# Optimization experiments

Measured on AMD Instinct MI355X. Metric: run time of the kernel, lower is better.

The kernel has to match this reference:

```python
import jax, jax.numpy as jnp
import numpy as np

D = 64
H = 4
HD = D // H
N_MOL, E_MOL = 2048, 32768
N_PROT, E_PROT = 8192, 262144
LN_EPS = 1e-5


def _lin_params(key, d_in, d_out):
    k1, k2 = jax.random.split(key)
    lim = 1.0 / np.sqrt(d_in)
    w = jax.random.uniform(k1, (d_in, d_out), minval=-lim, maxval=lim, dtype=jnp.float32)
    b = jax.random.uniform(k2, (d_out,), minval=-lim, maxval=lim, dtype=jnp.float32)
    return w, b


def setup_inputs() -> dict:
    key = jax.random.key(0)
    ks = jax.random.split(key, 20)
    inp = {
        'x_mol': jax.random.normal(ks[0], (N_MOL, D), dtype=jnp.float32),
        'edge_index_mol': jax.random.randint(ks[1], (2, E_MOL), 0, N_MOL),
        'edge_attr_mol': jax.random.normal(ks[2], (E_MOL, D), dtype=jnp.float32),
        'x_prot': jax.random.normal(ks[3], (N_PROT, D), dtype=jnp.float32),
        'edge_index_prot': jax.random.randint(ks[4], (2, E_PROT), 0, N_PROT),
        'edge_attr_prot': jax.random.normal(ks[5], (E_PROT, D), dtype=jnp.float32),
    }
    # GINE MLPs: Linear -> ReLU -> Linear
    inp['mol_w1'], inp['mol_b1'] = _lin_params(ks[6], D, D)
    inp['mol_w2'], inp['mol_b2'] = _lin_params(ks[7], D, D)
    inp['prot_w1'], inp['prot_b1'] = _lin_params(ks[8], D, D)
    inp['prot_w2'], inp['prot_b2'] = _lin_params(ks[9], D, D)
    # cross-attn mol->prot (query=mol, key/value=prot)
    inp['mp_wq'], inp['mp_bq'] = _lin_params(ks[10], D, D)
    inp['mp_wk'], inp['mp_bk'] = _lin_params(ks[11], D, D)
    inp['mp_wv'], inp['mp_bv'] = _lin_params(ks[12], D, D)
    # cross-attn prot->mol (query=prot, key/value=mol)
    inp['pm_wq'], inp['pm_bq'] = _lin_params(ks[13], D, D)
    inp['pm_wk'], inp['pm_bk'] = _lin_params(ks[14], D, D)
    inp['pm_wv'], inp['pm_bv'] = _lin_params(ks[15], D, D)
    # layer norms
    inp['ln_mol_g'] = jnp.ones((D,), jnp.float32)
    inp['ln_mol_b'] = jnp.zeros((D,), jnp.float32)
    inp['ln_prot_g'] = jnp.ones((D,), jnp.float32)
    inp['ln_prot_b'] = jnp.zeros((D,), jnp.float32)
    return inp


def _gine_conv(x, edge_index, edge_attr, w1, b1, w2, b2, n_nodes):
    # message: relu(x_j + edge_attr); aggregate: mean at target; update: MLP((1+eps)*x + aggr), eps=0
    src, dst = edge_index[0], edge_index[1]
    msg = jax.nn.relu(x[src] + edge_attr)                       # [E, D]
    ssum = jax.ops.segment_sum(msg, dst, num_segments=n_nodes)  # [N, D]
    cnt = jax.ops.segment_sum(jnp.ones((msg.shape[0],), msg.dtype), dst, num_segments=n_nodes)
    aggr = ssum / jnp.maximum(cnt, 1.0)[:, None]
    h = x + aggr
    h = jax.nn.relu(h @ w1 + b1) @ w2 + b2
    return h


def _cross_attn(q_nodes, k_nodes, wq, bq, wk, bk, wv, bv):
    Nq, Nk = q_nodes.shape[0], k_nodes.shape[0]
    Q = (q_nodes @ wq + bq).reshape(Nq, H, HD)
    K = (k_nodes @ wk + bk).reshape(Nk, H, HD)
    V = (k_nodes @ wv + bv).reshape(Nk, H, HD)
    scores = jnp.einsum('qhd,khd->hqk', Q, K) / np.sqrt(HD).astype(np.float32)
    attn = jax.nn.softmax(scores, axis=-1)                      # [H, Nq, Nk]
    out = jnp.einsum('hqk,khd->qhd', attn, V).reshape(Nq, D)
    return out


def _layer_norm(x, g, b):
    mu = jnp.mean(x, axis=-1, keepdims=True)
    var = jnp.mean(jnp.square(x - mu), axis=-1, keepdims=True)
    return (x - mu) * jax.lax.rsqrt(var + LN_EPS) * g + b


def reference(x_mol, edge_index_mol, edge_attr_mol, x_prot, edge_index_prot, edge_attr_prot,
              mol_w1, mol_b1, mol_w2, mol_b2, prot_w1, prot_b1, prot_w2, prot_b2,
              mp_wq, mp_bq, mp_wk, mp_bk, mp_wv, mp_bv,
              pm_wq, pm_bq, pm_wk, pm_bk, pm_wv, pm_bv,
              ln_mol_g, ln_mol_b, ln_prot_g, ln_prot_b):
    h_mol = jax.nn.relu(_gine_conv(x_mol, edge_index_mol, edge_attr_mol,
                                   mol_w1, mol_b1, mol_w2, mol_b2, x_mol.shape[0]))
    h_prot = jax.nn.relu(_gine_conv(x_prot, edge_index_prot, edge_attr_prot,
                                    prot_w1, prot_b1, prot_w2, prot_b2, x_prot.shape[0]))
    h_mol_attn = _cross_attn(h_mol, h_prot, mp_wq, mp_bq, mp_wk, mp_bk, mp_wv, mp_bv)
    h_prot_attn = _cross_attn(h_prot, h_mol, pm_wq, pm_bq, pm_wk, pm_bk, pm_wv, pm_bv)
    out_mol = _layer_norm(h_mol + h_mol_attn, ln_mol_g, ln_mol_b)
    out_prot = _layer_norm(h_prot + h_prot_attn, ln_prot_g, ln_prot_b)
    return out_mol, out_prot
```

## Files before the change

### kernel.cpp

```cpp
#include <hip/hip_runtime.h>

#define NM 2048
#define EM 32768
#define NP 8192
#define EP 262144

typedef __attribute__((ext_vector_type(8))) short short8;
typedef __attribute__((ext_vector_type(4))) float f32x4;

#define LOG2E 1.44269504088896340736f

__device__ __forceinline__ float e2(float x) { return __builtin_amdgcn_exp2f(x); }
__device__ __forceinline__ unsigned int pk_bf16_tr(float a, float b) {
    return __builtin_amdgcn_perm(__float_as_uint(a), __float_as_uint(b), 0x03020706u);
}
__device__ __forceinline__ unsigned short cvt_bf16(float f) {
    unsigned int u = __float_as_uint(f);
    u = (u + 0x7fff + ((u >> 16) & 1)) >> 16;
    return (unsigned short)u;
}

__global__ __launch_bounds__(256) void hist_kernel(
    const int* __restrict__ ei_m, const int* __restrict__ ei_p,
    int* __restrict__ cnt_m, int* __restrict__ cnt_p)
{
    int idx = blockIdx.x * 256 + threadIdx.x;
    if (idx < EM) atomicAdd(&cnt_m[ei_m[EM + idx]], 1);
    int j = idx - EM;
    if (j >= 0 && j < EP) atomicAdd(&cnt_p[ei_p[EP + j]], 1);
}

__global__ __launch_bounds__(256) void scan_kernel(
    const int* __restrict__ cnt_m, const int* __restrict__ cnt_p,
    int* __restrict__ start_m, int* __restrict__ start_p,
    int* __restrict__ cur_m, int* __restrict__ cur_p)
{
    const int* cnt; int* start; int* cur; int n;
    if (blockIdx.x == 0) { cnt = cnt_m; start = start_m; cur = cur_m; n = NM; }
    else                 { cnt = cnt_p; start = start_p; cur = cur_p; n = NP; }
    int per = n >> 8;
    int tid = threadIdx.x;
    int base = tid * per;
    int s = 0;
    for (int i = 0; i < per; i++) s += cnt[base + i];
    __shared__ int wsum[4];
    int lane = tid & 63, w = tid >> 6;
    int v = s;
    #pragma unroll
    for (int off = 1; off < 64; off <<= 1) {
        int u = __shfl_up(v, off, 64);
        if (lane >= off) v += u;
    }
    if (lane == 63) wsum[w] = v;
    __syncthreads();
    int wo = 0;
    for (int i = 0; i < w; i++) wo += wsum[i];
    int run = wo + v - s;
    for (int i = 0; i < per; i++) {
        start[base + i] = run; cur[base + i] = run;
        run += cnt[base + i];
    }
    if (tid == 255) start[n] = run;
}

__global__ __launch_bounds__(256) void scatter_kernel(
    const int* __restrict__ ei_m, const int* __restrict__ ei_p,
    int* __restrict__ cur_m, int* __restrict__ cur_p,
    int* __restrict__ pidx_m, int* __restrict__ pidx_p)
{
    int idx = blockIdx.x * 256 + threadIdx.x;
    if (idx < EM) {
        int d = ei_m[EM + idx];
        int pos = atomicAdd(&cur_m[d], 1);
        pidx_m[pos] = (idx << 11) | ei_m[idx];
    }
    int j = idx - EM;
    if (j >= 0 && j < EP) {
        int d = ei_p[EP + j];
        int pos = atomicAdd(&cur_p[d], 1);
        pidx_p[pos] = (j << 13) | ei_p[j];
    }
}

__global__ __launch_bounds__(256) void node_aggr_kernel(
    const float* __restrict__ x_m, const float* __restrict__ ea_m,
    const int* __restrict__ start_m, const int* __restrict__ pidx_m,
    const float* __restrict__ x_p, const float* __restrict__ ea_p,
    const int* __restrict__ start_p, const int* __restrict__ pidx_p,
    float* __restrict__ h0_m, float* __restrict__ h0_p)
{
    int wave = threadIdx.x >> 6, lane = threadIdx.x & 63;
    int nid = blockIdx.x * 4 + wave;
    const float *x, *ea; const int *start, *pidx; float* h0; int n, sh, msk;
    if (nid < NM) { x = x_m; ea = ea_m; start = start_m; pidx = pidx_m; h0 = h0_m; n = nid; sh = 11; msk = 2047; }
    else          { x = x_p; ea = ea_p; start = start_p; pidx = pidx_p; h0 = h0_p; n = nid - NM; sh = 13; msk = 8191; }
    int b  = __builtin_amdgcn_readfirstlane(start[n]);
    int e  = __builtin_amdgcn_readfirstlane(start[n + 1]);
    int deg = e - b;
    const int* pp = pidx + b;
    float acc = 0.f;
    int j = 0;
    for (; j + 8 <= deg; j += 8) {
        int v0 = __builtin_amdgcn_readfirstlane(pp[j]);
        int v1 = __builtin_amdgcn_readfirstlane(pp[j + 1]);
        int v2 = __builtin_amdgcn_readfirstlane(pp[j + 2]);
        int v3 = __builtin_amdgcn_readfirstlane(pp[j + 3]);
        int v4 = __builtin_amdgcn_readfirstlane(pp[j + 4]);
        int v5 = __builtin_amdgcn_readfirstlane(pp[j + 5]);
        int v6 = __builtin_amdgcn_readfirstlane(pp[j + 6]);
        int v7 = __builtin_amdgcn_readfirstlane(pp[j + 7]);
        float a0 = ea[(size_t)(((unsigned)v0) >> sh) * 64 + lane];
        float a1 = ea[(size_t)(((unsigned)v1) >> sh) * 64 + lane];
        float a2 = ea[(size_t)(((unsigned)v2) >> sh) * 64 + lane];
        float a3 = ea[(size_t)(((unsigned)v3) >> sh) * 64 + lane];
        float a4 = ea[(size_t)(((unsigned)v4) >> sh) * 64 + lane];
        float a5 = ea[(size_t)(((unsigned)v5) >> sh) * 64 + lane];
        float a6 = ea[(size_t)(((unsigned)v6) >> sh) * 64 + lane];
        float a7 = ea[(size_t)(((unsigned)v7) >> sh) * 64 + lane];
        float y0 = x[(size_t)(v0 & msk) * 64 + lane];
        float y1 = x[(size_t)(v1 & msk) * 64 + lane];
        float y2 = x[(size_t)(v2 & msk) * 64 + lane];
        float y3 = x[(size_t)(v3 & msk) * 64 + lane];
        float y4 = x[(size_t)(v4 & msk) * 64 + lane];
        float y5 = x[(size_t)(v5 & msk) * 64 + lane];
        float y6 = x[(size_t)(v6 & msk) * 64 + lane];
        float y7 = x[(size_t)(v7 & msk) * 64 + lane];
        acc += fmaxf(y0 + a0, 0.f); acc += fmaxf(y1 + a1, 0.f);
        acc += fmaxf(y2 + a2, 0.f); acc += fmaxf(y3 + a3, 0.f);
        acc += fmaxf(y4 + a4, 0.f); acc += fmaxf(y5 + a5, 0.f);
        acc += fmaxf(y6 + a6, 0.f); acc += fmaxf(y7 + a7, 0.f);
    }
    for (; j < deg; ++j) {
        int v0 = __builtin_amdgcn_readfirstlane(pp[j]);
        acc += fmaxf(x[(size_t)(v0 & msk) * 64 + lane] + ea[(size_t)(((unsigned)v0) >> sh) * 64 + lane], 0.f);
    }
    float aggr = acc / fmaxf((float)deg, 1.f);
    h0[(size_t)n * 64 + lane] = x[(size_t)n * 64 + lane] + aggr;
}

__global__ __launch_bounds__(256) void mlp_qkv_kernel(
    const float* __restrict__ h0_m, const float* __restrict__ h0_p,
    const float* __restrict__ w1m, const float* __restrict__ b1m,
    const float* __restrict__ w2m, const float* __restrict__ b2m,
    const float* __restrict__ w1p, const float* __restrict__ b1p,
    const float* __restrict__ w2p, const float* __restrict__ b2p,
    const float* __restrict__ wq_m, const float* __restrict__ bq_m,
    const float* __restrict__ wk_m, const float* __restrict__ bk_m,
    const float* __restrict__ wv_m, const float* __restrict__ bv_m,
    const float* __restrict__ wq_p, const float* __restrict__ bq_p,
    const float* __restrict__ wk_p, const float* __restrict__ bk_p,
    const float* __restrict__ wv_p, const float* __restrict__ bv_p,
    float* __restrict__ hm, float* __restrict__ hp,
    unsigned short* __restrict__ Qm, unsigned short* __restrict__ Km, unsigned short* __restrict__ Vtm,
    unsigned short* __restrict__ Qp, unsigned short* __restrict__ Kp, unsigned short* __restrict__ Vtp,
    int* __restrict__ norms)
{
    const float *h0, *w1, *b1, *w2, *b2, *wq, *bq, *wk, *bk, *wv, *bv;
    float* hout; unsigned short *Q, *K, *Vt; int row0, N, nbase;
    if (blockIdx.x < NM / 16) {
        h0 = h0_m; w1 = w1m; b1 = b1m; w2 = w2m; b2 = b2m;
        wq = wq_m; bq = bq_m; wk = wk_m; bk = bk_m; wv = wv_m; bv = bv_m;
        hout = hm; Q = Qm; K = Km; Vt = Vtm; N = NM; row0 = blockIdx.x * 16; nbase = 0;
    } else {
        h0 = h0_p; w1 = w1p; b1 = b1p; w2 = w2p; b2 = b2p;
        wq = wq_p; bq = bq_p; wk = wk_p; bk = bk_p; wv = wv_p; bv = bv_p;
        hout = hp; Q = Qp; K = Kp; Vt = Vtp; N = NP; row0 = (blockIdx.x - NM / 16) * 16; nbase = 2;
    }
    __shared__ float sWa[4096], sWb[4096], sWc[4096];
    __shared__ float sb1[64], sb2[64], sbq[64], sbk[64], sbv[64];
    __shared__ float sh0[16][64], sh1[16][64];
    __shared__ float rmx[8];
    int t = threadIdx.x;
    for (int i = t; i < 4096; i += 256) { sWa[i] = w1[i]; sWb[i] = w2[i]; sWc[i] = wq[i]; }
    if (t < 64) { sb1[t] = b1[t]; sb2[t] = b2[t]; sbq[t] = bq[t]; sbk[t] = bk[t]; sbv[t] = bv[t]; }
    for (int i = t; i < 16 * 64; i += 256) {
        int r = i >> 6, c = i & 63;
        sh0[r][c] = h0[(size_t)(row0 + r) * 64 + c];
    }
    __syncthreads();
    int j = t & 63, rs = t >> 6;
    for (int r = rs; r < 16; r += 4) {
        float a = sb1[j];
        #pragma unroll
        for (int c = 0; c < 64; c++) a += sh0[r][c] * sWa[c * 64 + j];
        sh1[r][j] = fmaxf(a, 0.0f);
    }
    __syncthreads();
    for (int r = rs; r < 16; r += 4) {
        float a = sb2[j];
        #pragma unroll
        for (int c = 0; c < 64; c++) a += sh1[r][c] * sWb[c * 64 + j];
        float hval = fmaxf(a, 0.0f);
        hout[(size_t)(row0 + r) * 64 + j] = hval;
        sh0[r][j] = hval;
    }
    for (int i = t; i < 4096; i += 256) sWa[i] = wk[i];
    __syncthreads();
    float qmx = 0.f, kmx = 0.f;
    for (int r = rs; r < 16; r += 4) {
        float aq = sbq[j], ak = sbk[j];
        #pragma unroll
        for (int c = 0; c < 64; c++) {
            float h = sh0[r][c];
            aq += h * sWc[c * 64 + j];
            ak += h * sWa[c * 64 + j];
        }
        float qs = aq * (0.25f * LOG2E);
        size_t o = (size_t)(row0 + r) * 64 + j;
        Q[o] = cvt_bf16(qs);
        K[o] = cvt_bf16(ak);
        float qsq = qs * qs, ksq = ak * ak;
        #pragma unroll
        for (int o2 = 1; o2 <= 8; o2 <<= 1) {
            qsq += __shfl_xor(qsq, o2, 64);
            ksq += __shfl_xor(ksq, o2, 64);
        }
        qmx = fmaxf(qmx, qsq);
        kmx = fmaxf(kmx, ksq);
    }
    for (int i = t; i < 4096; i += 256) sWb[i] = wv[i];
    qmx = fmaxf(qmx, __shfl_xor(qmx, 16, 64)); qmx = fmaxf(qmx, __shfl_xor(qmx, 32, 64));
    kmx = fmaxf(kmx, __shfl_xor(kmx, 16, 64)); kmx = fmaxf(kmx, __shfl_xor(kmx, 32, 64));
    if (j == 0) { rmx[rs] = qmx; rmx[4 + rs] = kmx; }
    __syncthreads();
    for (int r = rs; r < 16; r += 4) {
        float av = sbv[j];
        #pragma unroll
        for (int c = 0; c < 64; c++) av += sh0[r][c] * sWb[c * 64 + j];
        Vt[(size_t)j * N + row0 + r] = cvt_bf16(av);
    }
    if (t == 0) {
        float q4 = fmaxf(fmaxf(rmx[0], rmx[1]), fmaxf(rmx[2], rmx[3]));
        float k4 = fmaxf(fmaxf(rmx[4], rmx[5]), fmaxf(rmx[6], rmx[7]));
        atomicMax(&norms[nbase],     __float_as_int(sqrtf(q4)));
        atomicMax(&norms[nbase + 1], __float_as_int(sqrtf(k4)));
    }
}

__global__ __launch_bounds__(256) void attn_kernel(
    const unsigned short* __restrict__ Qm, const unsigned short* __restrict__ Km,
    const unsigned short* __restrict__ Vtm,
    const unsigned short* __restrict__ Qp, const unsigned short* __restrict__ Kp,
    const unsigned short* __restrict__ Vtp,
    const int* __restrict__ norms, float* __restrict__ partial)
{
    __shared__ unsigned int plds[4][2][2][16][20];
    int t = threadIdx.x;
    int wave = t >> 6;
    int lane = t & 63;
    int qrow = lane & 15;
    int quad = lane >> 4;
    int W = blockIdx.x * 4 + wave;

    const unsigned short *Q, *K, *Vt; int Nk; float m;
    int chunk, h, qt2, Tbase, T1off;
    if (W < 2048) {
        Q = Qm; K = Kp; Vt = Vtp; Nk = NP;
        m = __int_as_float(norms[0]) * __int_as_float(norms[3]);
        chunk = W & 7; h = (W >> 3) & 3; qt2 = W >> 5;
        Tbase = W + qt2 * 32; T1off = 32;
    } else {
        int W2 = W - 2048;
        Q = Qp; K = Km; Vt = Vtm; Nk = NM;
        m = __int_as_float(norms[2]) * __int_as_float(norms[1]);
        chunk = W2 & 1; h = (W2 >> 1) & 3; qt2 = W2 >> 3;
        Tbase = 4096 + W2 + qt2 * 8; T1off = 8;
    }

    short8 qfA = {}, qfB = {};
    if (quad < 2) {
        qfA = *(const short8*)(Q + ((size_t)(qt2 * 32 + qrow)) * 64 + h * 16 + quad * 8);
        qfB = *(const short8*)(Q + ((size_t)(qt2 * 32 + 16 + qrow)) * 64 + h * 16 + quad * 8);
    }

    const f32x4 zero4 = {0.f, 0.f, 0.f, 0.f};
    int kbase = chunk * 1024;
    const unsigned short* krow = K + (size_t)(kbase + qrow) * 64 + h * 16 + quad * 8;
    const unsigned short* vrow = Vt + ((size_t)(h * 16 + qrow)) * Nk + kbase + quad * 8;

    float lA = 0.0f, lB = 0.0f;
    f32x4 accA = zero4, accB = zero4;

    short8 kf0_0, kf1_0, vf_0, kf0_1, kf1_1, vf_1;
    kf0_0 = (short8){}; kf1_0 = (short8){};
    kf0_1 = (short8){}; kf1_1 = (short8){};
    if (quad < 2) {
        kf0_0 = *(const short8*)(krow);
        kf1_0 = *(const short8*)(krow + 16 * 64);
        kf0_1 = *(const short8*)(krow + 32 * 64);
        kf1_1 = *(const short8*)(krow + 48 * 64);
    }
    vf_0 = *(const short8*)(vrow);
    vf_1 = *(const short8*)(vrow + 32);

    short8 vf_prev;

#define QK_PHASE(IT, SLOT, BUF)                                                             \
    {                                                                                       \
        short8 kf0 = kf0_##SLOT, kf1 = kf1_##SLOT, vf = vf_##SLOT;                          \
        if ((IT) < 30) {                                                                    \
            int off = ((IT) + 2) * 32;                                                      \
            if (quad < 2) {                                                                 \
                kf0_##SLOT = *(const short8*)(krow + (size_t)off * 64);                     \
                kf1_##SLOT = *(const short8*)(krow + (size_t)(off + 16) * 64);              \
            }                                                                               \
            vf_##SLOT = *(const short8*)(vrow + off);                                       \
        }                                                                                   \
        f32x4 s0A = __builtin_amdgcn_mfma_f32_16x16x32_bf16(kf0, qfA, zero4, 0, 0, 0);      \
        f32x4 s1A = __builtin_amdgcn_mfma_f32_16x16x32_bf16(kf1, qfA, zero4, 0, 0, 0);      \
        f32x4 s0B = __builtin_amdgcn_mfma_f32_16x16x32_bf16(kf0, qfB, zero4, 0, 0, 0);      \
        f32x4 s1B = __builtin_amdgcn_mfma_f32_16x16x32_bf16(kf1, qfB, zero4, 0, 0, 0);      \
        float a00 = e2(s0A.x - m), a01 = e2(s0A.y - m), a02 = e2(s0A.z - m), a03 = e2(s0A.w - m); \
        float a10 = e2(s1A.x - m), a11 = e2(s1A.y - m), a12 = e2(s1A.z - m), a13 = e2(s1A.w - m); \
        float b00 = e2(s0B.x - m), b01 = e2(s0B.y - m), b02 = e2(s0B.z - m), b03 = e2(s0B.w - m); \
        float b10 = e2(s1B.x - m), b11 = e2(s1B.y - m), b12 = e2(s1B.z - m), b13 = e2(s1B.w - m); \
        lA += (((a00 + a01) + (a02 + a03)) + ((a10 + a11) + (a12 + a13)));                  \
        lB += (((b00 + b01) + (b02 + b03)) + ((b10 + b11) + (b12 + b13)));                  \
        uint2 wA0; wA0.x = pk_bf16_tr(a00, a01); wA0.y = pk_bf16_tr(a02, a03);              \
        uint2 wA1; wA1.x = pk_bf16_tr(a10, a11); wA1.y = pk_bf16_tr(a12, a13);              \
        uint2 wB0; wB0.x = pk_bf16_tr(b00, b01); wB0.y = pk_bf16_tr(b02, b03);              \
        uint2 wB1; wB1.x = pk_bf16_tr(b10, b11); wB1.y = pk_bf16_tr(b12, b13);              \
        *(uint2*)&plds[wave][0][BUF][qrow][quad * 2] = wA0;                                 \
        *(uint2*)&plds[wave][0][BUF][qrow][8 + quad * 2] = wA1;                             \
        *(uint2*)&plds[wave][1][BUF][qrow][quad * 2] = wB0;                                 \
        *(uint2*)&plds[wave][1][BUF][qrow][8 + quad * 2] = wB1;                             \
        vf_cur = vf;                                                                        \
    }

#define STEP(IT, SLOT, BUF, PREV)                                                           \
    {                                                                                       \
        short8 pfA = *(short8*)&plds[wave][0][PREV][qrow][quad * 4];                        \
        short8 pfB = *(short8*)&plds[wave][1][PREV][qrow][quad * 4];                        \
        short8 vf_cur;                                                                      \
        QK_PHASE(IT, SLOT, BUF)                                                             \
        accA = __builtin_amdgcn_mfma_f32_16x16x32_bf16(vf_prev, pfA, accA, 0, 0, 0);        \
        accB = __builtin_amdgcn_mfma_f32_16x16x32_bf16(vf_prev, pfB, accB, 0, 0, 0);        \
        vf_prev = vf_cur;                                                                   \
    }

    {
        short8 vf_cur;
        QK_PHASE(0, 0, 0)
        vf_prev = vf_cur;
    }
    for (int p = 0; p < 15; ++p) {
        int it1 = 2 * p + 1;
        STEP(it1, 1, 1, 0)
        STEP(it1 + 1, 0, 0, 1)
    }
    STEP(31, 1, 1, 0)
    {
        short8 pfA = *(short8*)&plds[wave][0][1][qrow][quad * 4];
        short8 pfB = *(short8*)&plds[wave][1][1][qrow][quad * 4];
        accA = __builtin_amdgcn_mfma_f32_16x16x32_bf16(vf_prev, pfA, accA, 0, 0, 0);
        accB = __builtin_amdgcn_mfma_f32_16x16x32_bf16(vf_prev, pfB, accB, 0, 0, 0);
    }
#undef STEP
#undef QK_PHASE

    float ltA = lA + __shfl_xor(lA, 16, 64); ltA += __shfl_xor(ltA, 32, 64);
    float ltB = lB + __shfl_xor(lB, 16, 64); ltB += __shfl_xor(ltB, 32, 64);

    float* pb0 = partial + (size_t)Tbase * 288;
    *(f32x4*)&pb0[qrow * 16 + quad * 4] = accA;
    if (quad == 0) pb0[272 + qrow] = ltA;
    float* pb1 = partial + (size_t)(Tbase + T1off) * 288;
    *(f32x4*)&pb1[qrow * 16 + quad * 4] = accB;
    if (quad == 0) pb1[272 + qrow] = ltB;
}

__global__ __launch_bounds__(256) void merge_ln_kernel(
    const float* __restrict__ partial,
    const float* __restrict__ h_m, const float* __restrict__ h_p,
    const float* __restrict__ gm, const float* __restrict__ bm,
    const float* __restrict__ gp, const float* __restrict__ bp_,
    float* __restrict__ out)
{
    int t = threadIdx.x;
    int grow = blockIdx.x * 4 + (t >> 6);
    int c = t & 63;
    const float *pbase, *hbuf, *g, *bb; float* o; int NC, row;
    if (grow < NM) { pbase = partial;               hbuf = h_m; g = gm; bb = bm;  o = out;             NC = 8; row = grow; }
    else           { pbase = partial + 4096 * 288;  hbuf = h_p; g = gp; bb = bp_; o = out + NM * 64;   NC = 2; row = grow - NM; }
    int hi = c >> 4, d = c & 15;
    int qt = row >> 4, ql = row & 15;
    const float* base = pbase + (size_t)(qt * 4 + hi) * NC * 288;
    float L = 0.0f, A = 0.0f;
    for (int cc = 0; cc < NC; ++cc) {
        L += base[cc * 288 + 272 + ql];
        A += base[cc * 288 + ql * 16 + d];
    }
    float v = hbuf[(size_t)row * 64 + c] + A / L;
    float s = v;
    #pragma unroll
    for (int o2 = 32; o2 >= 1; o2 >>= 1) s += __shfl_xor(s, o2, 64);
    float mu = s * (1.0f / 64.0f);
    float dv = v - mu;
    float sq = dv * dv;
    #pragma unroll
    for (int o2 = 32; o2 >= 1; o2 >>= 1) sq += __shfl_xor(sq, o2, 64);
    float var = sq * (1.0f / 64.0f);
    o[(size_t)row * 64 + c] = dv * rsqrtf(var + 1e-5f) * g[c] + bb[c];
}

extern "C" void kernel_launch(void* const* d_in, const int* in_sizes, int n_in,
                              void* d_out, int out_size, void* d_ws, size_t ws_size,
                              hipStream_t stream)
{
    const float* x_mol   = (const float*)d_in[0];
    const int*   ei_mol  = (const int*)  d_in[1];
    const float* ea_mol  = (const float*)d_in[2];
    const float* x_prot  = (const float*)d_in[3];
    const int*   ei_prot = (const int*)  d_in[4];
    const float* ea_prot = (const float*)d_in[5];
    const float* mol_w1  = (const float*)d_in[6];
    const float* mol_b1  = (const float*)d_in[7];
    const float* mol_w2  = (const float*)d_in[8];
    const float* mol_b2  = (const float*)d_in[9];
    const float* prot_w1 = (const float*)d_in[10];
    const float* prot_b1 = (const float*)d_in[11];
    const float* prot_w2 = (const float*)d_in[12];
    const float* prot_b2 = (const float*)d_in[13];
    const float* mp_wq = (const float*)d_in[14]; const float* mp_bq = (const float*)d_in[15];
    const float* mp_wk = (const float*)d_in[16]; const float* mp_bk = (const float*)d_in[17];
    const float* mp_wv = (const float*)d_in[18]; const float* mp_bv = (const float*)d_in[19];
    const float* pm_wq = (const float*)d_in[20]; const float* pm_bq = (const float*)d_in[21];
    const float* pm_wk = (const float*)d_in[22]; const float* pm_bk = (const float*)d_in[23];
    const float* pm_wv = (const float*)d_in[24]; const float* pm_bv = (const float*)d_in[25];
    const float* ln_mol_g  = (const float*)d_in[26];
    const float* ln_mol_b  = (const float*)d_in[27];
    const float* ln_prot_g = (const float*)d_in[28];
    const float* ln_prot_b = (const float*)d_in[29];

    float* ws = (float*)d_ws;
    float* h_mol   = ws;
    float* h_prot  = h_mol + 131072;
    float* partial = h_prot + 524288;
    float* h0_mol  = partial;
    float* h0_prot = h0_mol + 131072;
    int* ip      = (int*)(partial + 2359296);
    int* cnt_m   = ip;
    int* cnt_p   = cnt_m + 2048;
    int* norms   = cnt_p + 8192;
    int* start_m = norms + 4;
    int* start_p = start_m + 2052;
    int* cur_m   = start_p + 8196;
    int* cur_p   = cur_m + 2048;
    int* pidx_m  = cur_p + 8192;
    int* pidx_p  = pidx_m + 32768;
    unsigned short* bf = (unsigned short*)(pidx_p + 262144);
    unsigned short* Qm  = bf;
    unsigned short* Km  = Qm + 131072;
    unsigned short* Vtm = Km + 131072;
    unsigned short* Qp  = Vtm + 131072;
    unsigned short* Kp  = Qp + 524288;
    unsigned short* Vtp = Kp + 524288;

    hipMemsetAsync(cnt_m, 0, (size_t)(2048 + 8192 + 4) * sizeof(int), stream);

    const int EB = (EM + EP) / 256;
    hist_kernel<<<EB, 256, 0, stream>>>(ei_mol, ei_prot, cnt_m, cnt_p);
    scan_kernel<<<2, 256, 0, stream>>>(cnt_m, cnt_p, start_m, start_p, cur_m, cur_p);
    scatter_kernel<<<EB, 256, 0, stream>>>(ei_mol, ei_prot, cur_m, cur_p, pidx_m, pidx_p);
    node_aggr_kernel<<<(NM + NP) / 4, 256, 0, stream>>>(
        x_mol, ea_mol, start_m, pidx_m,
        x_prot, ea_prot, start_p, pidx_p, h0_mol, h0_prot);

    mlp_qkv_kernel<<<(NM + NP) / 16, 256, 0, stream>>>(
        h0_mol, h0_prot,
        mol_w1, mol_b1, mol_w2, mol_b2, prot_w1, prot_b1, prot_w2, prot_b2,
        mp_wq, mp_bq, pm_wk, pm_bk, pm_wv, pm_bv,
        pm_wq, pm_bq, mp_wk, mp_bk, mp_wv, mp_bv,
        h_mol, h_prot, Qm, Km, Vtm, Qp, Kp, Vtp, norms);

    attn_kernel<<<1024, 256, 0, stream>>>(Qm, Km, Vtm, Qp, Kp, Vtp, norms, partial);

    float* out = (float*)d_out;
    merge_ln_kernel<<<(NM + NP) / 4, 256, 0, stream>>>(
        partial, h_mol, h_prot, ln_mol_g, ln_mol_b, ln_prot_g, ln_prot_b, out);
}
```

Measured before the change: 303.5 us.

## Use 32x32x16 MFMA for attention scores and double rows per MLP block

The QK^T score computation in the attention kernel now uses one 32x32x16 bf16 MFMA per step in place of four 16x16x32 MFMAs. This also removes the idle half-wave loads for Q and K, and the P tiles are written to LDS in a new layout. Separately, the MLP/QKV kernel now handles 32 rows per block, so weight loads into shared memory are amortized over more rows. The trade-off is fewer blocks, more shared memory per block, and a remapped, more error-prone layout for the score rows and the row-sum reduction.

```diff
diff --git a/kernel.cpp b/kernel.cpp
--- a/kernel.cpp
+++ b/kernel.cpp
@@ -7,6 +7,7 @@
 
 typedef __attribute__((ext_vector_type(8))) short short8;
 typedef __attribute__((ext_vector_type(4))) float f32x4;
+typedef __attribute__((ext_vector_type(16))) float f32x16;
 
 #define LOG2E 1.44269504088896340736f
 
@@ -157,36 +158,36 @@
 {
     const float *h0, *w1, *b1, *w2, *b2, *wq, *bq, *wk, *bk, *wv, *bv;
     float* hout; unsigned short *Q, *K, *Vt; int row0, N, nbase;
-    if (blockIdx.x < NM / 16) {
+    if (blockIdx.x < NM / 32) {
         h0 = h0_m; w1 = w1m; b1 = b1m; w2 = w2m; b2 = b2m;
         wq = wq_m; bq = bq_m; wk = wk_m; bk = bk_m; wv = wv_m; bv = bv_m;
-        hout = hm; Q = Qm; K = Km; Vt = Vtm; N = NM; row0 = blockIdx.x * 16; nbase = 0;
+        hout = hm; Q = Qm; K = Km; Vt = Vtm; N = NM; row0 = blockIdx.x * 32; nbase = 0;
     } else {
         h0 = h0_p; w1 = w1p; b1 = b1p; w2 = w2p; b2 = b2p;
         wq = wq_p; bq = bq_p; wk = wk_p; bk = bk_p; wv = wv_p; bv = bv_p;
-        hout = hp; Q = Qp; K = Kp; Vt = Vtp; N = NP; row0 = (blockIdx.x - NM / 16) * 16; nbase = 2;
+        hout = hp; Q = Qp; K = Kp; Vt = Vtp; N = NP; row0 = (blockIdx.x - NM / 32) * 32; nbase = 2;
     }
     __shared__ float sWa[4096], sWb[4096], sWc[4096];
     __shared__ float sb1[64], sb2[64], sbq[64], sbk[64], sbv[64];
-    __shared__ float sh0[16][64], sh1[16][64];
+    __shared__ float sh0[32][64], sh1[32][64];
     __shared__ float rmx[8];
     int t = threadIdx.x;
     for (int i = t; i < 4096; i += 256) { sWa[i] = w1[i]; sWb[i] = w2[i]; sWc[i] = wq[i]; }
     if (t < 64) { sb1[t] = b1[t]; sb2[t] = b2[t]; sbq[t] = bq[t]; sbk[t] = bk[t]; sbv[t] = bv[t]; }
-    for (int i = t; i < 16 * 64; i += 256) {
+    for (int i = t; i < 32 * 64; i += 256) {
         int r = i >> 6, c = i & 63;
         sh0[r][c] = h0[(size_t)(row0 + r) * 64 + c];
     }
     __syncthreads();
     int j = t & 63, rs = t >> 6;
-    for (int r = rs; r < 16; r += 4) {
+    for (int r = rs; r < 32; r += 4) {
         float a = sb1[j];
         #pragma unroll
         for (int c = 0; c < 64; c++) a += sh0[r][c] * sWa[c * 64 + j];
         sh1[r][j] = fmaxf(a, 0.0f);
     }
     __syncthreads();
-    for (int r = rs; r < 16; r += 4) {
+    for (int r = rs; r < 32; r += 4) {
         float a = sb2[j];
         #pragma unroll
         for (int c = 0; c < 64; c++) a += sh1[r][c] * sWb[c * 64 + j];
@@ -197,7 +198,7 @@
     for (int i = t; i < 4096; i += 256) sWa[i] = wk[i];
     __syncthreads();
     float qmx = 0.f, kmx = 0.f;
-    for (int r = rs; r < 16; r += 4) {
+    for (int r = rs; r < 32; r += 4) {
         float aq = sbq[j], ak = sbk[j];
         #pragma unroll
         for (int c = 0; c < 64; c++) {
@@ -223,7 +224,7 @@
     kmx = fmaxf(kmx, __shfl_xor(kmx, 16, 64)); kmx = fmaxf(kmx, __shfl_xor(kmx, 32, 64));
     if (j == 0) { rmx[rs] = qmx; rmx[4 + rs] = kmx; }
     __syncthreads();
-    for (int r = rs; r < 16; r += 4) {
+    for (int r = rs; r < 32; r += 4) {
         float av = sbv[j];
         #pragma unroll
         for (int c = 0; c < 64; c++) av += sh0[r][c] * sWb[c * 64 + j];
@@ -250,6 +251,10 @@
     int lane = t & 63;
     int qrow = lane & 15;
     int quad = lane >> 4;
+    int q5   = lane & 31;
+    int half = lane >> 5;
+    int qtl  = q5 >> 4;
+    int dwb  = half * 2;
     int W = blockIdx.x * 4 + wave;
 
     const unsigned short *Q, *K, *Vt; int Nk; float m;
@@ -267,29 +272,20 @@
         Tbase = 4096 + W2 + qt2 * 8; T1off = 8;
     }
 
-    short8 qfA = {}, qfB = {};
-    if (quad < 2) {
-        qfA = *(const short8*)(Q + ((size_t)(qt2 * 32 + qrow)) * 64 + h * 16 + quad * 8);
-        qfB = *(const short8*)(Q + ((size_t)(qt2 * 32 + 16 + qrow)) * 64 + h * 16 + quad * 8);
-    }
-
+    short8 qf = *(const short8*)(Q + ((size_t)(qt2 * 32 + q5)) * 64 + h * 16 + half * 8);
+
+    const f32x16 zero16 = {0.f,0.f,0.f,0.f,0.f,0.f,0.f,0.f,0.f,0.f,0.f,0.f,0.f,0.f,0.f,0.f};
     const f32x4 zero4 = {0.f, 0.f, 0.f, 0.f};
     int kbase = chunk * 1024;
-    const unsigned short* krow = K + (size_t)(kbase + qrow) * 64 + h * 16 + quad * 8;
+    const unsigned short* krow = K + (size_t)(kbase + q5) * 64 + h * 16 + half * 8;
     const unsigned short* vrow = Vt + ((size_t)(h * 16 + qrow)) * Nk + kbase + quad * 8;
 
-    float lA = 0.0f, lB = 0.0f;
+    float l = 0.0f;
     f32x4 accA = zero4, accB = zero4;
 
-    short8 kf0_0, kf1_0, vf_0, kf0_1, kf1_1, vf_1;
-    kf0_0 = (short8){}; kf1_0 = (short8){};
-    kf0_1 = (short8){}; kf1_1 = (short8){};
-    if (quad < 2) {
-        kf0_0 = *(const short8*)(krow);
-        kf1_0 = *(const short8*)(krow + 16 * 64);
-        kf0_1 = *(const short8*)(krow + 32 * 64);
-        kf1_1 = *(const short8*)(krow + 48 * 64);
-    }
+    short8 kf_0, kf_1, vf_0, vf_1;
+    kf_0 = *(const short8*)(krow);
+    kf_1 = *(const short8*)(krow + 32 * 64);
     vf_0 = *(const short8*)(vrow);
     vf_1 = *(const short8*)(vrow + 32);
 
@@ -297,33 +293,27 @@
 
 #define QK_PHASE(IT, SLOT, BUF)                                                             \
     {                                                                                       \
-        short8 kf0 = kf0_##SLOT, kf1 = kf1_##SLOT, vf = vf_##SLOT;                          \
+        short8 kf = kf_##SLOT; short8 vf = vf_##SLOT;                                       \
         if ((IT) < 30) {                                                                    \
             int off = ((IT) + 2) * 32;                                                      \
-            if (quad < 2) {                                                                 \
-                kf0_##SLOT = *(const short8*)(krow + (size_t)off * 64);                     \
-                kf1_##SLOT = *(const short8*)(krow + (size_t)(off + 16) * 64);              \
-            }                                                                               \
+            kf_##SLOT = *(const short8*)(krow + (size_t)off * 64);                          \
             vf_##SLOT = *(const short8*)(vrow + off);                                       \
         }                                                                                   \
-        f32x4 s0A = __builtin_amdgcn_mfma_f32_16x16x32_bf16(kf0, qfA, zero4, 0, 0, 0);      \
-        f32x4 s1A = __builtin_amdgcn_mfma_f32_16x16x32_bf16(kf1, qfA, zero4, 0, 0, 0);      \
-        f32x4 s0B = __builtin_amdgcn_mfma_f32_16x16x32_bf16(kf0, qfB, zero4, 0, 0, 0);      \
-        f32x4 s1B = __builtin_amdgcn_mfma_f32_16x16x32_bf16(kf1, qfB, zero4, 0, 0, 0);      \
-        float a00 = e2(s0A.x - m), a01 = e2(s0A.y - m), a02 = e2(s0A.z - m), a03 = e2(s0A.w - m); \
-        float a10 = e2(s1A.x - m), a11 = e2(s1A.y - m), a12 = e2(s1A.z - m), a13 = e2(s1A.w - m); \
-        float b00 = e2(s0B.x - m), b01 = e2(s0B.y - m), b02 = e2(s0B.z - m), b03 = e2(s0B.w - m); \
-        float b10 = e2(s1B.x - m), b11 = e2(s1B.y - m), b12 = e2(s1B.z - m), b13 = e2(s1B.w - m); \
-        lA += (((a00 + a01) + (a02 + a03)) + ((a10 + a11) + (a12 + a13)));                  \
-        lB += (((b00 + b01) + (b02 + b03)) + ((b10 + b11) + (b12 + b13)));                  \
-        uint2 wA0; wA0.x = pk_bf16_tr(a00, a01); wA0.y = pk_bf16_tr(a02, a03);              \
-        uint2 wA1; wA1.x = pk_bf16_tr(a10, a11); wA1.y = pk_bf16_tr(a12, a13);              \
-        uint2 wB0; wB0.x = pk_bf16_tr(b00, b01); wB0.y = pk_bf16_tr(b02, b03);              \
-        uint2 wB1; wB1.x = pk_bf16_tr(b10, b11); wB1.y = pk_bf16_tr(b12, b13);              \
-        *(uint2*)&plds[wave][0][BUF][qrow][quad * 2] = wA0;                                 \
-        *(uint2*)&plds[wave][0][BUF][qrow][8 + quad * 2] = wA1;                             \
-        *(uint2*)&plds[wave][1][BUF][qrow][quad * 2] = wB0;                                 \
-        *(uint2*)&plds[wave][1][BUF][qrow][8 + quad * 2] = wB1;                             \
+        f32x16 s = __builtin_amdgcn_mfma_f32_32x32x16_bf16(kf, qf, zero16, 0, 0, 0);        \
+        float p0  = e2(s[0] - m),  p1  = e2(s[1] - m),  p2  = e2(s[2] - m),  p3  = e2(s[3] - m);  \
+        float p4  = e2(s[4] - m),  p5  = e2(s[5] - m),  p6  = e2(s[6] - m),  p7  = e2(s[7] - m);  \
+        float p8  = e2(s[8] - m),  p9  = e2(s[9] - m),  p10 = e2(s[10] - m), p11 = e2(s[11] - m); \
+        float p12 = e2(s[12] - m), p13 = e2(s[13] - m), p14 = e2(s[14] - m), p15 = e2(s[15] - m); \
+        l += (((p0 + p1) + (p2 + p3)) + ((p4 + p5) + (p6 + p7)))                            \
+           + (((p8 + p9) + (p10 + p11)) + ((p12 + p13) + (p14 + p15)));                     \
+        uint2 w0; w0.x = pk_bf16_tr(p0, p1);   w0.y = pk_bf16_tr(p2, p3);                   \
+        uint2 w1; w1.x = pk_bf16_tr(p4, p5);   w1.y = pk_bf16_tr(p6, p7);                   \
+        uint2 w2; w2.x = pk_bf16_tr(p8, p9);   w2.y = pk_bf16_tr(p10, p11);                 \
+        uint2 w3; w3.x = pk_bf16_tr(p12, p13); w3.y = pk_bf16_tr(p14, p15);                 \
+        *(uint2*)&plds[wave][qtl][BUF][qrow][dwb]      = w0;                                \
+        *(uint2*)&plds[wave][qtl][BUF][qrow][dwb + 4]  = w1;                                \
+        *(uint2*)&plds[wave][qtl][BUF][qrow][dwb + 8]  = w2;                                \
+        *(uint2*)&plds[wave][qtl][BUF][qrow][dwb + 12] = w3;                                \
         vf_cur = vf;                                                                        \
     }
 
@@ -344,9 +334,8 @@
         vf_prev = vf_cur;
     }
     for (int p = 0; p < 15; ++p) {
-        int it1 = 2 * p + 1;
-        STEP(it1, 1, 1, 0)
-        STEP(it1 + 1, 0, 0, 1)
+        STEP(2 * p + 1, 1, 1, 0)
+        STEP(2 * p + 2, 0, 0, 1)
     }
     STEP(31, 1, 1, 0)
     {
@@ -358,15 +347,14 @@
 #undef STEP
 #undef QK_PHASE
 
-    float ltA = lA + __shfl_xor(lA, 16, 64); ltA += __shfl_xor(ltA, 32, 64);
-    float ltB = lB + __shfl_xor(lB, 16, 64); ltB += __shfl_xor(ltB, 32, 64);
+    float ltot = l + __shfl_xor(l, 32, 64);
 
     float* pb0 = partial + (size_t)Tbase * 288;
     *(f32x4*)&pb0[qrow * 16 + quad * 4] = accA;
-    if (quad == 0) pb0[272 + qrow] = ltA;
     float* pb1 = partial + (size_t)(Tbase + T1off) * 288;
     *(f32x4*)&pb1[qrow * 16 + quad * 4] = accB;
-    if (quad == 0) pb1[272 + qrow] = ltB;
+    if (lane < 16)       pb0[272 + q5] = ltot;
+    else if (lane < 32)  pb1[272 + (q5 - 16)] = ltot;
 }
 
 __global__ __launch_bounds__(256) void merge_ln_kernel(
@@ -466,7 +454,7 @@
         x_mol, ea_mol, start_m, pidx_m,
         x_prot, ea_prot, start_p, pidx_p, h0_mol, h0_prot);
 
-    mlp_qkv_kernel<<<(NM + NP) / 16, 256, 0, stream>>>(
+    mlp_qkv_kernel<<<(NM + NP) / 32, 256, 0, stream>>>(
         h0_mol, h0_prot,
         mol_w1, mol_b1, mol_w2, mol_b2, prot_w1, prot_b1, prot_w2, prot_b2,
         mp_wq, mp_bq, pm_wk, pm_bk, pm_wv, pm_bv,
```

Measured after the change: 294.1 us. 3.1% less time.
